# Kernel optimization log

Measured on AMD Instinct MI355X. Metric: run time of the kernel, lower is better.

## Reference

```python
import jax, jax.numpy as jnp
import numpy as np

V, D, NL, K, B, L, FF = 32000, 512, 4, 32, 2, 1024, 2048


def _ln(x, g, b, eps=1e-5):
    m = jnp.mean(x, axis=-1, keepdims=True)
    v = jnp.mean((x - m) ** 2, axis=-1, keepdims=True)
    return (x - m) * jax.lax.rsqrt(v + eps) * g + b


def setup_inputs() -> dict:
    key = jax.random.key(0)
    ks = jax.random.split(key, 16)
    s = 0.02
    n = lambda k, shape: jax.random.normal(k, shape, jnp.float32) * s
    inp = {
        "tokens": jax.random.randint(ks[0], (B, L), 0, V),
        "embed": n(ks[1], (V, D)),
        "ln1_g": jnp.ones((NL, D)), "ln1_b": jnp.zeros((NL, D)),
        "cp_w1": n(ks[2], (NL, D, D)), "cp_b1": jnp.zeros((NL, D)),
        "cp_w2": n(ks[3], (NL, D, K)), "cp_b2": jnp.zeros((NL, K)),
        "pos_scale": 0.5 * jnp.ones((NL,)), "content_scale": 0.5 * jnp.ones((NL,)),
        "val_w": n(ks[4], (NL, D, D)), "val_b": jnp.zeros((NL, D)),
        "oln_g": jnp.ones((NL, D)), "oln_b": jnp.zeros((NL, D)),
        "out_w": n(ks[5], (NL, D, D)), "out_b": jnp.zeros((NL, D)),
        "ln2_g": jnp.ones((NL, D)), "ln2_b": jnp.zeros((NL, D)),
        "ffn_w1": n(ks[6], (NL, D, FF)), "ffn_b1": jnp.zeros((NL, FF)),
        "ffn_w2": n(ks[7], (NL, FF, D)), "ffn_b2": jnp.zeros((NL, D)),
        "no_g": jnp.ones((D,)), "no_b": jnp.zeros((D,)),
        "head_b": jnp.zeros((V,)),
    }
    return inp


def _forward(tokens, embed, ln1_g, ln1_b, cp_w1, cp_b1, cp_w2, cp_b2,
             pos_scale, content_scale, val_w, val_b, oln_g, oln_b, out_w, out_b,
             ln2_g, ln2_b, ffn_w1, ffn_b1, ffn_w2, ffn_b2, no_g, no_b, head_b):
    Bn, Ln = tokens.shape
    Kn = cp_b2.shape[1]
    # fixed positional phases (register_buffer in torch)
    freqs = 1.0 / 10000.0 ** (jnp.arange(Kn, dtype=jnp.float32) / Kn)
    pos_phase = jnp.arange(Ln, dtype=jnp.float32)[:, None] * freqs[None, :]  # [L,K]
    inv_norm = 1.0 / jnp.sqrt(jnp.arange(1, Ln + 1, dtype=jnp.float32) * Kn)[None, :, None]
    h = embed[tokens]  # [B,L,D]
    for i in range(ln1_g.shape[0]):
        # --- DualAddressingPhasor on normed input ---
        x = _ln(h, ln1_g[i], ln1_b[i])
        cp = jnp.tanh(jnp.tanh(x @ cp_w1[i] + cp_b1[i]) @ cp_w2[i] + cp_b2[i]) * jnp.pi  # [B,L,K]
        tp = pos_scale[i] * pos_phase[None] + content_scale[i] * cp
        v = x @ val_w[i] + val_b[i]  # [B,L,D]
        c, s_ = jnp.cos(tp), jnp.sin(tp)  # [B,L,K]
        mem_r = jnp.cumsum(c[..., None] * v[:, :, None, :], axis=1)  # [B,L,K,D]
        mem_i = jnp.cumsum(s_[..., None] * v[:, :, None, :], axis=1)
        retrieved = (jnp.einsum('blkd,blk->bld', mem_r, c)
                     + jnp.einsum('blkd,blk->bld', mem_i, s_)) * inv_norm
        # phasor returns x + to_out(retrieved); block adds it back to h
        h = h + x + (_ln(retrieved, oln_g[i], oln_b[i]) @ out_w[i] + out_b[i])
        # --- FFN ---
        y = _ln(h, ln2_g[i], ln2_b[i])
        h = h + jax.nn.gelu(y @ ffn_w1[i] + ffn_b1[i], approximate=False) @ ffn_w2[i] + ffn_b2[i]
    # tied output head: head.weight = embed.weight
    return _ln(h, no_g, no_b) @ embed.T + head_b


def reference(tokens, embed, ln1_g, ln1_b, cp_w1, cp_b1, cp_w2, cp_b2,
              pos_scale, content_scale, val_w, val_b, oln_g, oln_b, out_w, out_b,
              ln2_g, ln2_b, ffn_w1, ffn_b1, ffn_w2, ffn_b2, no_g, no_b, head_b):
    return _forward(tokens, embed, ln1_g, ln1_b, cp_w1, cp_b1, cp_w2, cp_b2,
                    pos_scale, content_scale, val_w, val_b, oln_g, oln_b, out_w, out_b,
                    ln2_g, ln2_b, ffn_w1, ffn_b1, ffn_w2, ffn_b2, no_g, no_b, head_b)
```

## Files before the change

kernel.cpp:

```cpp
#include <hip/hip_runtime.h>
#include <hip/hip_bf16.h>
#include <math.h>

#define V_  32000
#define D_  512
#define NL_ 4
#define K_  32
#define B_  2
#define L_  1024
#define FF_ 2048
#define MR_ (B_ * L_)

typedef __bf16 bf16_t;
typedef __bf16 bf16x8 __attribute__((ext_vector_type(8)));
typedef float  f32x4  __attribute__((ext_vector_type(4)));

#define FLAG_TANH   1
#define FLAG_GELU   2
#define FLAG_INV    8
#define FLAG_CAUSAL 16

#define GLDS(gsrc, ldst) \
  __builtin_amdgcn_global_load_lds( \
      (const __attribute__((address_space(1))) unsigned int*)(const void*)(gsrc), \
      (__attribute__((address_space(3))) unsigned int*)(void*)(ldst), 16, 0, 0)

__global__ void gather_kernel(const int* __restrict__ tokens,
                              const float* __restrict__ embed,
                              float* __restrict__ h) {
    int row = blockIdx.x;
    int t = tokens[row];
    const float4* src = (const float4*)(embed + (size_t)t * D_);
    float4* dst = (float4*)(h + (size_t)row * D_);
    dst[threadIdx.x] = src[threadIdx.x];
}

__global__ __launch_bounds__(256) void cvt_kernel(const float* __restrict__ in,
                                                  bf16_t* __restrict__ out) {
    size_t i = ((size_t)blockIdx.x * 256 + threadIdx.x) * 8;
    float4 f0 = ((const float4*)(in + i))[0];
    float4 f1 = ((const float4*)(in + i))[1];
    bf16x8 ov;
    ov[0] = (bf16_t)f0.x; ov[1] = (bf16_t)f0.y;
    ov[2] = (bf16_t)f0.z; ov[3] = (bf16_t)f0.w;
    ov[4] = (bf16_t)f1.x; ov[5] = (bf16_t)f1.y;
    ov[6] = (bf16_t)f1.z; ov[7] = (bf16_t)f1.w;
    *(bf16x8*)(out + i) = ov;
}

__global__ __launch_bounds__(256) void ln_kernel(const float* __restrict__ in,
                                                 const float* __restrict__ g,
                                                 const float* __restrict__ b,
                                                 float* __restrict__ outf,
                                                 bf16_t* __restrict__ outb) {
    int row = blockIdx.x, tid = threadIdx.x;
    const float* rp = in + (size_t)row * D_;
    float v0 = rp[tid], v1 = rp[tid + 256];
    float s = v0 + v1, q = v0 * v0 + v1 * v1;
#pragma unroll
    for (int o = 32; o > 0; o >>= 1) {
        s += __shfl_down(s, o, 64);
        q += __shfl_down(q, o, 64);
    }
    __shared__ float ss[4], sq[4];
    if ((tid & 63) == 0) { ss[tid >> 6] = s; sq[tid >> 6] = q; }
    __syncthreads();
    float ts = ss[0] + ss[1] + ss[2] + ss[3];
    float tq = sq[0] + sq[1] + sq[2] + sq[3];
    float mean = ts * (1.0f / D_);
    float var = tq * (1.0f / D_) - mean * mean;
    float rstd = rsqrtf(var + 1e-5f);
    float o0 = (v0 - mean) * rstd * g[tid] + b[tid];
    float o1 = (v1 - mean) * rstd * g[tid + 256] + b[tid + 256];
    if (outf) {
        outf[(size_t)row * D_ + tid]       = o0;
        outf[(size_t)row * D_ + tid + 256] = o1;
    }
    if (outb) {
        outb[(size_t)row * D_ + tid]       = (bf16_t)o0;
        outb[(size_t)row * D_ + tid + 256] = (bf16_t)o1;
    }
}

__global__ __launch_bounds__(256) void tconv_kernel(const float* __restrict__ in,
                                                    bf16_t* __restrict__ out,
                                                    int R, int C,
                                                    size_t inz, size_t outz) {
    __shared__ float t[32][33];
    const float* ip = in + (size_t)blockIdx.z * inz;
    bf16_t* op = out + (size_t)blockIdx.z * outz;
    int r0 = blockIdx.y * 32, c0 = blockIdx.x * 32;
    int tx = threadIdx.x & 31, ty = threadIdx.x >> 5;
#pragma unroll
    for (int rr = 0; rr < 4; ++rr)
        t[ty + rr * 8][tx] = ip[(size_t)(r0 + ty + rr * 8) * C + c0 + tx];
    __syncthreads();
#pragma unroll
    for (int rr = 0; rr < 4; ++rr)
        op[(size_t)(c0 + ty + rr * 8) * R + r0 + tx] = (bf16_t)t[tx][ty + rr * 8];
}

template<int BM, int BN, bool BF32>
__global__ __launch_bounds__(256) void mgemm(
    const bf16_t* __restrict__ A, const void* __restrict__ Bp,
    const float* __restrict__ bias, const float* __restrict__ res1,
    const float* __restrict__ res2, float* __restrict__ Cf,
    bf16_t* __restrict__ Cb, int M, int N, int Kd, int flags,
    long long strA, long long strB, long long strC, int swz) {
    constexpr int NBUF = 4;
    __shared__ bf16_t sA[NBUF][BM * 32];
    __shared__ bf16_t sB[NBUF][BN * 32];
    const int tid = threadIdx.x;
    const int wave = tid >> 6, lane = tid & 63;
    const int lrow = lane & 15, quad = lane >> 4;
    int bx = blockIdx.x, by = blockIdx.y;
    if (swz) {
        int gx = gridDim.x, gy = gridDim.y;
        int nwg = gx * gy;
        int lid = by * gx + bx;
        int q = nwg >> 3, r = nwg & 7;
        int xcd = lid & 7, slot = lid >> 3;
        int base = (xcd < r) ? xcd * (q + 1) : r * (q + 1) + (xcd - r) * q;
        int nid = base + slot;
        bx = nid / gy;
        by = nid - bx * gy;
    }
    const int m0 = by * BM, n0 = bx * BN;
    const int z = blockIdx.z;
    A += (size_t)z * strA;
    const bf16_t* Bb = (const bf16_t*)Bp + (BF32 ? 0 : (size_t)z * strB);
    const float*  Bf = (const float*)Bp  + (BF32 ? (size_t)z * strB : 0);
    constexpr int TM = BM / 32, TN = BN / 32;
    const int wm = (wave >> 1) * (BM / 2), wn = (wave & 1) * (BN / 2);
    f32x4 acc[TM][TN] = {};

    if constexpr (BF32) {
        for (int k0 = 0; k0 < Kd; k0 += 32) {
#pragma unroll
            for (int rb = 0; rb < BM / 64; ++rb) {
                int rowblk = wave * (BM / 64) + rb;
                int ml = rowblk * 16 + (lane >> 2);
                int qs = (lane & 3) ^ ((ml >> 1) & 3);
                GLDS(A + (size_t)(m0 + ml) * Kd + k0 + qs * 8, &sA[0][rowblk * 512]);
            }
#pragma unroll
            for (int rb = 0; rb < (BN * 4) / 256; ++rb) {
                int s = rb * 256 + tid;
                int nl = s >> 2, ql = s & 3;
                int qs = ql ^ ((nl >> 1) & 3);
                const float* src = Bf + (size_t)(n0 + nl) * Kd + k0 + qs * 8;
                float4 f0 = ((const float4*)src)[0];
                float4 f1 = ((const float4*)src)[1];
                bf16x8 ov;
                ov[0] = (bf16_t)f0.x; ov[1] = (bf16_t)f0.y;
                ov[2] = (bf16_t)f0.z; ov[3] = (bf16_t)f0.w;
                ov[4] = (bf16_t)f1.x; ov[5] = (bf16_t)f1.y;
                ov[6] = (bf16_t)f1.z; ov[7] = (bf16_t)f1.w;
                *(bf16x8*)(&sB[0][s * 8]) = ov;
            }
            __syncthreads();
            bf16x8 af[TM], bv[TN];
#pragma unroll
            for (int i = 0; i < TM; ++i) {
                int row = wm + i * 16 + lrow;
                af[i] = *(const bf16x8*)(&sA[0][(row * 4 + (quad ^ ((row >> 1) & 3))) * 8]);
            }
#pragma unroll
            for (int j = 0; j < TN; ++j) {
                int rown = wn + j * 16 + lrow;
                bv[j] = *(const bf16x8*)(&sB[0][(rown * 4 + (quad ^ ((rown >> 1) & 3))) * 8]);
            }
#pragma unroll
            for (int i = 0; i < TM; ++i)
#pragma unroll
                for (int j = 0; j < TN; ++j)
                    acc[i][j] = __builtin_amdgcn_mfma_f32_16x16x32_bf16(af[i], bv[j], acc[i][j], 0, 0, 0);
            __syncthreads();
        }
    } else {
        int kend = Kd;
        if (flags & FLAG_CAUSAL) { int ke = m0 + BM; kend = ke < Kd ? ke : Kd; }
        const int nk = kend >> 5;
        constexpr int NLD = BM / 64 + BN / 64;
        auto stage = [&](int t) {
            const int buf = t & (NBUF - 1);
            const int k0 = t << 5;
#pragma unroll
            for (int rb = 0; rb < BM / 64; ++rb) {
                int rowblk = wave * (BM / 64) + rb;
                int ml = rowblk * 16 + (lane >> 2);
                int qs = (lane & 3) ^ ((ml >> 1) & 3);
                GLDS(A + (size_t)(m0 + ml) * Kd + k0 + qs * 8, &sA[buf][rowblk * 512]);
            }
#pragma unroll
            for (int rb = 0; rb < BN / 64; ++rb) {
                int rowblk = wave * (BN / 64) + rb;
                int nl = rowblk * 16 + (lane >> 2);
                int qs = (lane & 3) ^ ((nl >> 1) & 3);
                GLDS(Bb + (size_t)(n0 + nl) * Kd + k0 + qs * 8, &sB[buf][rowblk * 512]);
            }
        };
        for (int t = 0; t < NBUF - 1 && t < nk; ++t) stage(t);
        for (int t = 0; t < nk; ++t) {
            const int nxt = t + NBUF - 1;
            if (nxt < nk) stage(nxt);
            const int issued_last = (nxt < nk) ? nxt : nk - 1;
            const int ahead = issued_last - t;
            if (ahead >= 3)      asm volatile("s_waitcnt vmcnt(%0)" :: "n"(3 * NLD) : "memory");
            else if (ahead == 2) asm volatile("s_waitcnt vmcnt(%0)" :: "n"(2 * NLD) : "memory");
            else if (ahead == 1) asm volatile("s_waitcnt vmcnt(%0)" :: "n"(1 * NLD) : "memory");
            else                 asm volatile("s_waitcnt vmcnt(0)" ::: "memory");
            __builtin_amdgcn_s_barrier();
            const int buf = t & (NBUF - 1);
            const bf16_t* sAc = sA[buf];
            const bf16_t* sBc = sB[buf];
            bf16x8 af[TM], bv[TN];
#pragma unroll
            for (int i = 0; i < TM; ++i) {
                int row = wm + i * 16 + lrow;
                af[i] = *(const bf16x8*)(sAc + (row * 4 + (quad ^ ((row >> 1) & 3))) * 8);
            }
#pragma unroll
            for (int j = 0; j < TN; ++j) {
                int rown = wn + j * 16 + lrow;
                bv[j] = *(const bf16x8*)(sBc + (rown * 4 + (quad ^ ((rown >> 1) & 3))) * 8);
            }
#pragma unroll
            for (int i = 0; i < TM; ++i)
#pragma unroll
                for (int j = 0; j < TN; ++j)
                    acc[i][j] = __builtin_amdgcn_mfma_f32_16x16x32_bf16(af[i], bv[j], acc[i][j], 0, 0, 0);
            asm volatile("s_waitcnt lgkmcnt(0)" ::: "memory");
            __builtin_amdgcn_s_barrier();
        }
    }

    const size_t zo = (size_t)z * strC;
#pragma unroll
    for (int i = 0; i < TM; ++i) {
#pragma unroll
        for (int reg = 0; reg < 4; ++reg) {
            int m = m0 + wm + i * 16 + quad * 4 + reg;
            float rs = (flags & FLAG_INV) ? rsqrtf((float)(m + 1) * (float)K_) : 1.0f;
#pragma unroll
            for (int j = 0; j < TN; ++j) {
                int n = n0 + wn + j * 16 + lrow;
                float vv = acc[i][j][reg];
                if (bias) vv += bias[n];
                vv *= rs;
                if (flags & FLAG_TANH) vv = tanhf(vv);
                else if (flags & FLAG_GELU) vv = 0.5f * vv * (1.0f + erff(vv * 0.7071067811865476f));
                size_t idx = zo + (size_t)m * N + n;
                if (res1) vv += res1[idx];
                if (res2) vv += res2[idx];
                if (Cf) Cf[idx] = vv;
                if (Cb) Cb[idx] = (bf16_t)vv;
            }
        }
    }
}

__global__ void phase_kernel(const float* __restrict__ t1,
                             const float* __restrict__ w2,
                             const float* __restrict__ b2,
                             const float* __restrict__ ps,
                             const float* __restrict__ cs,
                             int layer,
                             float* __restrict__ cbuf,
                             float* __restrict__ sbuf) {
    int row = blockIdx.x;
    int l = row & (L_ - 1);
    int tid = threadIdx.x;
    int k = tid & 31, hh = tid >> 5;
    const float* tr = t1 + (size_t)row * D_;
    float acc = 0.f;
    for (int d = hh * 256; d < hh * 256 + 256; ++d)
        acc = fmaf(tr[d], w2[d * K_ + k], acc);
    __shared__ float red[64];
    red[tid] = acc;
    __syncthreads();
    if (hh == 0) {
        float zz = red[k] + red[k + 32] + b2[k];
        float cp = tanhf(zz) * 3.14159265358979323846f;
        float freq = expf(-(float)k * (9.210340371976184f / (float)K_));
        float tp = ps[layer] * (float)l * freq + cs[layer] * cp;
        cbuf[(size_t)row * K_ + k] = cosf(tp);
        sbuf[(size_t)row * K_ + k] = sinf(tp);
    }
}

__global__ __launch_bounds__(256) void score_kernel(const float* __restrict__ cbuf,
                                                    const float* __restrict__ sbuf,
                                                    bf16_t* __restrict__ Ab) {
    int b = blockIdx.z;
    int l0 = blockIdx.y * 16, j0 = blockIdx.x * 16;
    if (j0 > l0) return;
    int tx = threadIdx.x, ty = threadIdx.y;
    int tid = ty * 16 + tx;
    __shared__ float Cl[16][33], Sl[16][33], Cj[16][33], Sj[16][33];
    const float* cb = cbuf + (size_t)b * L_ * K_;
    const float* sb = sbuf + (size_t)b * L_ * K_;
    for (int q = tid; q < 16 * 32; q += 256) {
        int rr = q >> 5, kk = q & 31;
        Cl[rr][kk] = cb[(size_t)(l0 + rr) * K_ + kk];
        Sl[rr][kk] = sb[(size_t)(l0 + rr) * K_ + kk];
        Cj[rr][kk] = cb[(size_t)(j0 + rr) * K_ + kk];
        Sj[rr][kk] = sb[(size_t)(j0 + rr) * K_ + kk];
    }
    __syncthreads();
    int l = l0 + ty, j = j0 + tx;
    float acc = 0.f;
#pragma unroll
    for (int kk = 0; kk < 32; ++kk)
        acc += Cl[ty][kk] * Cj[tx][kk] + Sl[ty][kk] * Sj[tx][kk];
    Ab[((size_t)b * L_ + l) * L_ + j] = (bf16_t)((j <= l) ? acc : 0.f);
}

extern "C" void kernel_launch(void* const* d_in, const int* in_sizes, int n_in,
                              void* d_out, int out_size, void* d_ws, size_t ws_size,
                              hipStream_t stream) {
    const int*   tokens        = (const int*)d_in[0];
    const float* embed         = (const float*)d_in[1];
    const float* ln1_g         = (const float*)d_in[2];
    const float* ln1_b         = (const float*)d_in[3];
    const float* cp_w1         = (const float*)d_in[4];
    const float* cp_b1         = (const float*)d_in[5];
    const float* cp_w2         = (const float*)d_in[6];
    const float* cp_b2         = (const float*)d_in[7];
    const float* pos_scale     = (const float*)d_in[8];
    const float* content_scale = (const float*)d_in[9];
    const float* val_w         = (const float*)d_in[10];
    const float* val_b         = (const float*)d_in[11];
    const float* oln_g         = (const float*)d_in[12];
    const float* oln_b         = (const float*)d_in[13];
    const float* out_w         = (const float*)d_in[14];
    const float* out_b         = (const float*)d_in[15];
    const float* ln2_g         = (const float*)d_in[16];
    const float* ln2_b         = (const float*)d_in[17];
    const float* ffn_w1        = (const float*)d_in[18];
    const float* ffn_b1        = (const float*)d_in[19];
    const float* ffn_w2        = (const float*)d_in[20];
    const float* ffn_b2        = (const float*)d_in[21];
    const float* no_g          = (const float*)d_in[22];
    const float* no_b          = (const float*)d_in[23];
    const float* head_b        = (const float*)d_in[24];
    float* out = (float*)d_out;

    float* h  = out;
    float* x  = h  + (size_t)MR_ * D_;
    float* t1 = x  + (size_t)MR_ * D_;
    float* v  = t1 + (size_t)MR_ * D_;
    float* r  = v  + (size_t)MR_ * D_;
    float* cb = r  + (size_t)MR_ * D_;
    float* sb = cb + (size_t)MR_ * K_;
    bf16_t* x_bf  = (bf16_t*)(sb + (size_t)MR_ * K_);
    bf16_t* r_bf  = x_bf  + (size_t)MR_ * D_;
    bf16_t* y_bf  = r_bf  + (size_t)MR_ * D_;
    bf16_t* ff_bf = y_bf  + (size_t)MR_ * D_;
    bf16_t* sc_bf = ff_bf + (size_t)MR_ * FF_;
    bf16_t* vT_bf = sc_bf + (size_t)B_ * L_ * L_;
    bf16_t* w1T   = vT_bf + (size_t)B_ * D_ * L_;
    bf16_t* vwT   = w1T   + (size_t)NL_ * D_ * D_;
    bf16_t* owT   = vwT   + (size_t)NL_ * D_ * D_;
    bf16_t* f1T   = owT   + (size_t)NL_ * D_ * D_;
    bf16_t* f2T   = f1T   + (size_t)NL_ * FF_ * D_;
    bf16_t* hn_bf = (bf16_t*)d_ws;
    bf16_t* emb_bf = hn_bf + (size_t)MR_ * D_;
    const bool big_ws =
        ws_size >= ((size_t)MR_ * D_ + (size_t)V_ * D_) * sizeof(bf16_t);

    gather_kernel<<<MR_, 128, 0, stream>>>(tokens, embed, h);

    tconv_kernel<<<dim3(16, 16, NL_), 256, 0, stream>>>(cp_w1, w1T, D_, D_, (size_t)D_ * D_, (size_t)D_ * D_);
    tconv_kernel<<<dim3(16, 16, NL_), 256, 0, stream>>>(val_w, vwT, D_, D_, (size_t)D_ * D_, (size_t)D_ * D_);
    tconv_kernel<<<dim3(16, 16, NL_), 256, 0, stream>>>(out_w, owT, D_, D_, (size_t)D_ * D_, (size_t)D_ * D_);
    tconv_kernel<<<dim3(64, 16, NL_), 256, 0, stream>>>(ffn_w1, f1T, D_, FF_, (size_t)D_ * FF_, (size_t)D_ * FF_);
    tconv_kernel<<<dim3(16, 64, NL_), 256, 0, stream>>>(ffn_w2, f2T, FF_, D_, (size_t)FF_ * D_, (size_t)FF_ * D_);
    if (big_ws)
        cvt_kernel<<<(V_ * D_) / 2048, 256, 0, stream>>>(embed, emb_bf);

    for (int i = 0; i < NL_; ++i) {
        ln_kernel<<<MR_, 256, 0, stream>>>(h, ln1_g + i * D_, ln1_b + i * D_, x, x_bf);
        mgemm<64, 64, false><<<dim3(8, 32, 1), 256, 0, stream>>>(
            x_bf, w1T + (size_t)i * D_ * D_, cp_b1 + i * D_,
            nullptr, nullptr, t1, nullptr, MR_, D_, D_, FLAG_TANH, 0, 0, 0, 1);
        phase_kernel<<<MR_, 64, 0, stream>>>(
            t1, cp_w2 + (size_t)i * D_ * K_, cp_b2 + i * K_,
            pos_scale, content_scale, i, cb, sb);
        mgemm<64, 64, false><<<dim3(8, 32, 1), 256, 0, stream>>>(
            x_bf, vwT + (size_t)i * D_ * D_, val_b + i * D_,
            nullptr, nullptr, v, nullptr, MR_, D_, D_, 0, 0, 0, 0, 1);
        tconv_kernel<<<dim3(16, 32, B_), 256, 0, stream>>>(
            v, vT_bf, L_, D_, (size_t)L_ * D_, (size_t)D_ * L_);
        score_kernel<<<dim3(L_ / 16, L_ / 16, B_), dim3(16, 16), 0, stream>>>(cb, sb, sc_bf);
        mgemm<64, 64, false><<<dim3(8, 16, B_), 256, 0, stream>>>(
            sc_bf, vT_bf, nullptr, nullptr, nullptr, r, nullptr,
            L_, D_, L_, FLAG_INV | FLAG_CAUSAL,
            (long long)L_ * L_, (long long)D_ * L_, (long long)L_ * D_, 1);
        ln_kernel<<<MR_, 256, 0, stream>>>(r, oln_g + i * D_, oln_b + i * D_, nullptr, r_bf);
        mgemm<64, 64, false><<<dim3(8, 32, 1), 256, 0, stream>>>(
            r_bf, owT + (size_t)i * D_ * D_, out_b + i * D_,
            h, x, h, nullptr, MR_, D_, D_, 0, 0, 0, 0, 1);
        ln_kernel<<<MR_, 256, 0, stream>>>(h, ln2_g + i * D_, ln2_b + i * D_, nullptr, y_bf);
        mgemm<128, 128, false><<<dim3(16, 16, 1), 256, 0, stream>>>(
            y_bf, f1T + (size_t)i * FF_ * D_, ffn_b1 + i * FF_,
            nullptr, nullptr, nullptr, ff_bf, MR_, FF_, D_, FLAG_GELU, 0, 0, 0, 1);
        mgemm<64, 64, false><<<dim3(8, 32, 1), 256, 0, stream>>>(
            ff_bf, f2T + (size_t)i * D_ * FF_, ffn_b2 + i * D_,
            h, nullptr, h, nullptr, MR_, D_, FF_, 0, 0, 0, 0, 1);
    }

    ln_kernel<<<MR_, 256, 0, stream>>>(h, no_g, no_b, nullptr, hn_bf);
    if (big_ws) {
        mgemm<128, 128, false><<<dim3(V_ / 128, MR_ / 128, 1), 256, 0, stream>>>(
            hn_bf, emb_bf, head_b, nullptr, nullptr, out, nullptr,
            MR_, V_, D_, 0, 0, 0, 0, 1);
    } else {
        mgemm<128, 128, true><<<dim3(V_ / 128, MR_ / 128, 1), 256, 0, stream>>>(
            hn_bf, embed, head_b, nullptr, nullptr, out, nullptr,
            MR_, V_, D_, 0, 0, 0, 0, 1);
    }
}
```

Measured before the change: 1.540 ms.

## Fuse content-phase and value projections into one GEMM; retune pipeline depth and head tile

The cp_w1 and val_w projections are concatenated into a single N=1024 GEMM with a concatenated bias. A new flag applies tanh only to the first half of the columns, so one launch replaces two and the normalized input is read once. The GEMM template now takes its buffer count as a parameter: the 64x64 GEMMs go to 8 stages and the vocabulary head uses a 128x256 tile with 2 stages, which changes LDS use, occupancy and wave count. The phase and transpose kernels are updated to read from the interleaved output with a doubled row stride.

```diff
diff --git a/kernel.cpp b/kernel.cpp
--- a/kernel.cpp
+++ b/kernel.cpp
@@ -19,6 +19,7 @@
 #define FLAG_GELU   2
 #define FLAG_INV    8
 #define FLAG_CAUSAL 16
+#define FLAG_TANHLO 32
 
 #define GLDS(gsrc, ldst) \
   __builtin_amdgcn_global_load_lds( \
@@ -46,6 +47,14 @@
     ov[4] = (bf16_t)f1.x; ov[5] = (bf16_t)f1.y;
     ov[6] = (bf16_t)f1.z; ov[7] = (bf16_t)f1.w;
     *(bf16x8*)(out + i) = ov;
+}
+
+__global__ void bconcat_kernel(const float* __restrict__ a,
+                               const float* __restrict__ b,
+                               float* __restrict__ o) {
+    int i = blockIdx.x, t = threadIdx.x;
+    o[(size_t)i * 2 * D_ + t]       = a[(size_t)i * D_ + t];
+    o[(size_t)i * 2 * D_ + D_ + t]  = b[(size_t)i * D_ + t];
 }
 
 __global__ __launch_bounds__(256) void ln_kernel(const float* __restrict__ in,
@@ -100,14 +109,13 @@
         op[(size_t)(c0 + ty + rr * 8) * R + r0 + tx] = (bf16_t)t[tx][ty + rr * 8];
 }
 
-template<int BM, int BN, bool BF32>
+template<int BM, int BN, int NBUF, bool BF32>
 __global__ __launch_bounds__(256) void mgemm(
     const bf16_t* __restrict__ A, const void* __restrict__ Bp,
     const float* __restrict__ bias, const float* __restrict__ res1,
     const float* __restrict__ res2, float* __restrict__ Cf,
     bf16_t* __restrict__ Cb, int M, int N, int Kd, int flags,
     long long strA, long long strB, long long strC, int swz) {
-    constexpr int NBUF = 4;
     __shared__ bf16_t sA[NBUF][BM * 32];
     __shared__ bf16_t sB[NBUF][BN * 32];
     const int tid = threadIdx.x;
@@ -206,10 +214,16 @@
             if (nxt < nk) stage(nxt);
             const int issued_last = (nxt < nk) ? nxt : nk - 1;
             const int ahead = issued_last - t;
-            if (ahead >= 3)      asm volatile("s_waitcnt vmcnt(%0)" :: "n"(3 * NLD) : "memory");
-            else if (ahead == 2) asm volatile("s_waitcnt vmcnt(%0)" :: "n"(2 * NLD) : "memory");
-            else if (ahead == 1) asm volatile("s_waitcnt vmcnt(%0)" :: "n"(1 * NLD) : "memory");
-            else                 asm volatile("s_waitcnt vmcnt(0)" ::: "memory");
+            switch (ahead) {
+              case 0: asm volatile("s_waitcnt vmcnt(0)" ::: "memory"); break;
+              case 1: asm volatile("s_waitcnt vmcnt(%0)" :: "n"(1 * NLD) : "memory"); break;
+              case 2: asm volatile("s_waitcnt vmcnt(%0)" :: "n"(2 * NLD) : "memory"); break;
+              case 3: asm volatile("s_waitcnt vmcnt(%0)" :: "n"(3 * NLD) : "memory"); break;
+              case 4: asm volatile("s_waitcnt vmcnt(%0)" :: "n"(4 * NLD) : "memory"); break;
+              case 5: asm volatile("s_waitcnt vmcnt(%0)" :: "n"(5 * NLD) : "memory"); break;
+              case 6: asm volatile("s_waitcnt vmcnt(%0)" :: "n"(6 * NLD) : "memory"); break;
+              default: asm volatile("s_waitcnt vmcnt(%0)" :: "n"(7 * NLD) : "memory"); break;
+            }
             __builtin_amdgcn_s_barrier();
             const int buf = t & (NBUF - 1);
             const bf16_t* sAc = sA[buf];
@@ -250,6 +264,7 @@
                 vv *= rs;
                 if (flags & FLAG_TANH) vv = tanhf(vv);
                 else if (flags & FLAG_GELU) vv = 0.5f * vv * (1.0f + erff(vv * 0.7071067811865476f));
+                else if (flags & FLAG_TANHLO) { if (n < D_) vv = tanhf(vv); }
                 size_t idx = zo + (size_t)m * N + n;
                 if (res1) vv += res1[idx];
                 if (res2) vv += res2[idx];
@@ -272,7 +287,7 @@
     int l = row & (L_ - 1);
     int tid = threadIdx.x;
     int k = tid & 31, hh = tid >> 5;
-    const float* tr = t1 + (size_t)row * D_;
+    const float* tr = t1 + (size_t)row * (2 * D_);
     float acc = 0.f;
     for (int d = hh * 256; d < hh * 256 + 256; ++d)
         acc = fmaf(tr[d], w2[d * K_ + k], acc);
@@ -346,24 +361,23 @@
     const float* head_b        = (const float*)d_in[24];
     float* out = (float*)d_out;
 
-    float* h  = out;
-    float* x  = h  + (size_t)MR_ * D_;
-    float* t1 = x  + (size_t)MR_ * D_;
-    float* v  = t1 + (size_t)MR_ * D_;
-    float* r  = v  + (size_t)MR_ * D_;
-    float* cb = r  + (size_t)MR_ * D_;
-    float* sb = cb + (size_t)MR_ * K_;
+    float* h   = out;
+    float* x   = h  + (size_t)MR_ * D_;
+    float* t1v = x  + (size_t)MR_ * D_;
+    float* r   = t1v + (size_t)MR_ * 2 * D_;
+    float* cb  = r  + (size_t)MR_ * D_;
+    float* sb  = cb + (size_t)MR_ * K_;
     bf16_t* x_bf  = (bf16_t*)(sb + (size_t)MR_ * K_);
     bf16_t* r_bf  = x_bf  + (size_t)MR_ * D_;
     bf16_t* y_bf  = r_bf  + (size_t)MR_ * D_;
     bf16_t* ff_bf = y_bf  + (size_t)MR_ * D_;
     bf16_t* sc_bf = ff_bf + (size_t)MR_ * FF_;
     bf16_t* vT_bf = sc_bf + (size_t)B_ * L_ * L_;
-    bf16_t* w1T   = vT_bf + (size_t)B_ * D_ * L_;
-    bf16_t* vwT   = w1T   + (size_t)NL_ * D_ * D_;
-    bf16_t* owT   = vwT   + (size_t)NL_ * D_ * D_;
+    bf16_t* wvT   = vT_bf + (size_t)B_ * D_ * L_;
+    bf16_t* owT   = wvT   + (size_t)NL_ * 2 * D_ * D_;
     bf16_t* f1T   = owT   + (size_t)NL_ * D_ * D_;
     bf16_t* f2T   = f1T   + (size_t)NL_ * FF_ * D_;
+    float*  b1v   = (float*)((((uintptr_t)(f2T + (size_t)NL_ * D_ * FF_)) + 15) & ~(uintptr_t)15);
     bf16_t* hn_bf = (bf16_t*)d_ws;
     bf16_t* emb_bf = hn_bf + (size_t)MR_ * D_;
     const bool big_ws =
@@ -371,8 +385,9 @@
 
     gather_kernel<<<MR_, 128, 0, stream>>>(tokens, embed, h);
 
-    tconv_kernel<<<dim3(16, 16, NL_), 256, 0, stream>>>(cp_w1, w1T, D_, D_, (size_t)D_ * D_, (size_t)D_ * D_);
-    tconv_kernel<<<dim3(16, 16, NL_), 256, 0, stream>>>(val_w, vwT, D_, D_, (size_t)D_ * D_, (size_t)D_ * D_);
+    tconv_kernel<<<dim3(16, 16, NL_), 256, 0, stream>>>(cp_w1, wvT, D_, D_, (size_t)D_ * D_, (size_t)2 * D_ * D_);
+    tconv_kernel<<<dim3(16, 16, NL_), 256, 0, stream>>>(val_w, wvT + (size_t)D_ * D_, D_, D_, (size_t)D_ * D_, (size_t)2 * D_ * D_);
+    bconcat_kernel<<<NL_, 512, 0, stream>>>(cp_b1, val_b, b1v);
     tconv_kernel<<<dim3(16, 16, NL_), 256, 0, stream>>>(out_w, owT, D_, D_, (size_t)D_ * D_, (size_t)D_ * D_);
     tconv_kernel<<<dim3(64, 16, NL_), 256, 0, stream>>>(ffn_w1, f1T, D_, FF_, (size_t)D_ * FF_, (size_t)D_ * FF_);
     tconv_kernel<<<dim3(16, 64, NL_), 256, 0, stream>>>(ffn_w2, f2T, FF_, D_, (size_t)FF_ * D_, (size_t)FF_ * D_);
@@ -381,42 +396,39 @@
 
     for (int i = 0; i < NL_; ++i) {
         ln_kernel<<<MR_, 256, 0, stream>>>(h, ln1_g + i * D_, ln1_b + i * D_, x, x_bf);
-        mgemm<64, 64, false><<<dim3(8, 32, 1), 256, 0, stream>>>(
-            x_bf, w1T + (size_t)i * D_ * D_, cp_b1 + i * D_,
-            nullptr, nullptr, t1, nullptr, MR_, D_, D_, FLAG_TANH, 0, 0, 0, 1);
+        mgemm<64, 64, 8, false><<<dim3(16, 32, 1), 256, 0, stream>>>(
+            x_bf, wvT + (size_t)i * 2 * D_ * D_, b1v + (size_t)i * 2 * D_,
+            nullptr, nullptr, t1v, nullptr, MR_, 2 * D_, D_, FLAG_TANHLO, 0, 0, 0, 1);
         phase_kernel<<<MR_, 64, 0, stream>>>(
-            t1, cp_w2 + (size_t)i * D_ * K_, cp_b2 + i * K_,
+            t1v, cp_w2 + (size_t)i * D_ * K_, cp_b2 + i * K_,
             pos_scale, content_scale, i, cb, sb);
-        mgemm<64, 64, false><<<dim3(8, 32, 1), 256, 0, stream>>>(
-            x_bf, vwT + (size_t)i * D_ * D_, val_b + i * D_,
-            nullptr, nullptr, v, nullptr, MR_, D_, D_, 0, 0, 0, 0, 1);
         tconv_kernel<<<dim3(16, 32, B_), 256, 0, stream>>>(
-            v, vT_bf, L_, D_, (size_t)L_ * D_, (size_t)D_ * L_);
+            t1v + D_, vT_bf, L_, 2 * D_, (size_t)L_ * 2 * D_, (size_t)D_ * L_);
         score_kernel<<<dim3(L_ / 16, L_ / 16, B_), dim3(16, 16), 0, stream>>>(cb, sb, sc_bf);
-        mgemm<64, 64, false><<<dim3(8, 16, B_), 256, 0, stream>>>(
+        mgemm<64, 64, 8, false><<<dim3(8, 16, B_), 256, 0, stream>>>(
             sc_bf, vT_bf, nullptr, nullptr, nullptr, r, nullptr,
             L_, D_, L_, FLAG_INV | FLAG_CAUSAL,
             (long long)L_ * L_, (long long)D_ * L_, (long long)L_ * D_, 1);
         ln_kernel<<<MR_, 256, 0, stream>>>(r, oln_g + i * D_, oln_b + i * D_, nullptr, r_bf);
-        mgemm<64, 64, false><<<dim3(8, 32, 1), 256, 0, stream>>>(
+        mgemm<64, 64, 8, false><<<dim3(8, 32, 1), 256, 0, stream>>>(
             r_bf, owT + (size_t)i * D_ * D_, out_b + i * D_,
             h, x, h, nullptr, MR_, D_, D_, 0, 0, 0, 0, 1);
         ln_kernel<<<MR_, 256, 0, stream>>>(h, ln2_g + i * D_, ln2_b + i * D_, nullptr, y_bf);
-        mgemm<128, 128, false><<<dim3(16, 16, 1), 256, 0, stream>>>(
+        mgemm<128, 128, 4, false><<<dim3(16, 16, 1), 256, 0, stream>>>(
             y_bf, f1T + (size_t)i * FF_ * D_, ffn_b1 + i * FF_,
             nullptr, nullptr, nullptr, ff_bf, MR_, FF_, D_, FLAG_GELU, 0, 0, 0, 1);
-        mgemm<64, 64, false><<<dim3(8, 32, 1), 256, 0, stream>>>(
+        mgemm<64, 64, 8, false><<<dim3(8, 32, 1), 256, 0, stream>>>(
             ff_bf, f2T + (size_t)i * D_ * FF_, ffn_b2 + i * D_,
             h, nullptr, h, nullptr, MR_, D_, FF_, 0, 0, 0, 0, 1);
     }
 
     ln_kernel<<<MR_, 256, 0, stream>>>(h, no_g, no_b, nullptr, hn_bf);
     if (big_ws) {
-        mgemm<128, 128, false><<<dim3(V_ / 128, MR_ / 128, 1), 256, 0, stream>>>(
+        mgemm<128, 256, 2, false><<<dim3(V_ / 256, MR_ / 128, 1), 256, 0, stream>>>(
             hn_bf, emb_bf, head_b, nullptr, nullptr, out, nullptr,
             MR_, V_, D_, 0, 0, 0, 0, 1);
     } else {
-        mgemm<128, 128, true><<<dim3(V_ / 128, MR_ / 128, 1), 256, 0, stream>>>(
+        mgemm<128, 128, 1, true><<<dim3(V_ / 128, MR_ / 128, 1), 256, 0, stream>>>(
             hn_bf, embed, head_b, nullptr, nullptr, out, nullptr,
             MR_, V_, D_, 0, 0, 0, 0, 1);
     }
```

Measured after the change: 1.911 ms. +24.1%, slower.
